# Optimization experiments

Hardware: AMD Instinct MI355X
Metric: run time of the kernel (lower is better)

## Reference

```python
import jax, jax.numpy as jnp
import numpy as np

WINDOW_SIZE = 11
SIGMA = 1.5
K2 = 0.03
PAD = WINDOW_SIZE // 2


def _gaussian_window(size, sigma):
    coords = np.arange(size, dtype=np.float32) - size // 2
    g = np.exp(-coords ** 2 / (2.0 * sigma ** 2))
    g = g / g.sum()
    w2d = np.outer(g, g)  # [size, size]
    return jnp.asarray(w2d[None, None], dtype=jnp.float32)  # [1,1,size,size]


def _blur(x, w):
    # x: [B,1,H,W], w: [1,1,k,k]; SAME zero padding, matches F.conv2d(padding=k//2)
    return jax.lax.conv_general_dilated(
        x, w, window_strides=(1, 1), padding=[(PAD, PAD), (PAD, PAD)],
        dimension_numbers=("NCHW", "OIHW", "NCHW"))


def setup_inputs() -> dict:
    key = jax.random.key(0)
    k1, k2 = jax.random.split(key)
    B, C, H, W = 32, 1, 512, 512
    inp = jax.random.uniform(k1, (B, C, H, W), dtype=jnp.float32)
    tgt = jax.random.uniform(k2, (B, C, H, W), dtype=jnp.float32)
    mask = jnp.ones((B, C, H, W), dtype=jnp.float32)
    window = _gaussian_window(WINDOW_SIZE, SIGMA)
    return {"input": inp, "target": tgt, "mask": mask, "window": window}


def reference(input, target, mask, window):
    # mask application (mask path is always exercised, matching the torch code)
    inp = input * mask
    tgt = target * mask

    mw = _blur(mask, window) + 1e-08  # blurred mask normalizer

    mu_i = _blur(inp, window) / mw
    mu_t = _blur(tgt, window) / mw

    sigma_i_sq = _blur(inp * inp, window) / mw - mu_i * mu_i
    sigma_t_sq = _blur(tgt * tgt, window) / mw - mu_t * mu_t
    sigma_it = _blur(inp * tgt, window) / mw - mu_i * mu_t

    L = jnp.maximum(jnp.max(inp), jnp.max(tgt))
    C2 = (K2 * L) ** 2
    C3 = C2 / 2.0

    sigma_i = jnp.sqrt(jax.nn.relu(sigma_i_sq) + 1e-12)
    sigma_t = jnp.sqrt(jax.nn.relu(sigma_t_sq) + 1e-12)

    structure_map = (sigma_it + C3) / (sigma_i * sigma_t + C3 + 1e-08)
    return 1.0 - jnp.mean(structure_map)
```

## Files before the change

### kernel.cpp

```cpp
#include <hip/hip_runtime.h>
#include <math.h>

#define H 512
#define W 512
#define TX 32
#define TY 32
#define SX 44
#define NPIX (32LL*512*512)

__device__ inline unsigned encf(float f) {
    unsigned u = __float_as_uint(f);
    return (u & 0x80000000u) ? ~u : (u | 0x80000000u);
}
__device__ inline float decf(unsigned e) {
    unsigned u = (e & 0x80000000u) ? (e ^ 0x80000000u) : ~e;
    return __uint_as_float(u);
}

__global__ __launch_bounds__(256) void maxred_kernel(
        const float* __restrict__ in, const float* __restrict__ tg,
        const float* __restrict__ mk, unsigned* __restrict__ mx) {
    const float4* in4 = (const float4*)in;
    const float4* tg4 = (const float4*)tg;
    const float4* mk4 = (const float4*)mk;
    long long n4 = NPIX / 4;
    long long idx = (long long)blockIdx.x * blockDim.x + threadIdx.x;
    long long stride = (long long)gridDim.x * blockDim.x;
    float ma = -INFINITY, mb = -INFINITY;
    for (long long i = idx; i < n4; i += stride) {
        float4 a = in4[i], b = tg4[i], c = mk4[i];
        ma = fmaxf(ma, fmaxf(fmaxf(a.x * c.x, a.y * c.y), fmaxf(a.z * c.z, a.w * c.w)));
        mb = fmaxf(mb, fmaxf(fmaxf(b.x * c.x, b.y * c.y), fmaxf(b.z * c.z, b.w * c.w)));
    }
    float m = fmaxf(ma, mb);
    #pragma unroll
    for (int off = 32; off; off >>= 1) m = fmaxf(m, __shfl_down(m, off, 64));
    __shared__ float smax[4];
    int lane = threadIdx.x & 63, wid = threadIdx.x >> 6;
    if (lane == 0) smax[wid] = m;
    __syncthreads();
    if (threadIdx.x == 0) {
        float r = fmaxf(fmaxf(smax[0], smax[1]), fmaxf(smax[2], smax[3]));
        atomicMax(mx, encf(r));
    }
}

__global__ __launch_bounds__(256, 4) void ssim_kernel(
        const float* __restrict__ in, const float* __restrict__ tg,
        const float* __restrict__ mk, const float* __restrict__ win,
        const unsigned* __restrict__ mxp, double* __restrict__ sum) {
    __shared__ __align__(16) float vch[6][TY][SX];
    __shared__ float gw[11];
    __shared__ float ssum[4];

    int t = threadIdx.x;
    if (t < 11) {
        float s = 0.f;
        #pragma unroll
        for (int j = 0; j < 11; j++) s += win[t * 11 + j];
        gw[t] = s;
    }
    float L = decf(*mxp);
    float C3 = 0.5f * (0.03f * L) * (0.03f * L);
    __syncthreads();

    float wk[11];
    #pragma unroll
    for (int k = 0; k < 11; k++)
        wk[k] = __uint_as_float(__builtin_amdgcn_readfirstlane(__float_as_uint(gw[k])));

    int img = blockIdx.z;
    int y0 = blockIdx.y * TY, x0 = blockIdx.x * TX;
    const size_t base = (size_t)img * H * W;
    const float* inb = in + base;
    const float* tgb = tg + base;
    const float* mkb = mk + base;

    if (t < 168) {
        int s = t / 42, cc = t - s * 42;
        int x = x0 - 5 + cc;
        bool inx = (unsigned)x < (unsigned)W;
        int xc = inx ? x : 0;
        float xs = inx ? 1.f : 0.f;
        int ybase = y0 + 8 * s - 5;
        float acc[6][8];
        #pragma unroll
        for (int ch = 0; ch < 6; ch++)
            #pragma unroll
            for (int u = 0; u < 8; u++) acc[ch][u] = 0.f;

        if (ybase >= 0 && ybase <= H - 18) {
            size_t g = (size_t)ybase * W + xc;
            #pragma unroll
            for (int j = 0; j < 18; j++) {
                float m = mkb[g], iv = inb[g], tv = tgb[g];
                g += W;
                float a = iv * m, b = tv * m;
                float v[6] = { m, a, b, a * a, b * b, a * b };
                #pragma unroll
                for (int u = 0; u < 8; u++) {
                    int k = j - u;
                    if (k >= 0 && k < 11) {
                        float w = wk[k];
                        #pragma unroll
                        for (int ch = 0; ch < 6; ch++)
                            acc[ch][u] = fmaf(w, v[ch], acc[ch][u]);
                    }
                }
            }
        } else {
            #pragma unroll
            for (int j = 0; j < 18; j++) {
                int y = ybase + j;
                bool yok = (unsigned)y < (unsigned)H;
                size_t g = (size_t)(yok ? y : 0) * W + xc;
                float sc = yok ? 1.f : 0.f;
                float m = mkb[g] * sc, iv = inb[g] * sc, tv = tgb[g] * sc;
                float a = iv * m, b = tv * m;
                float v[6] = { m, a, b, a * a, b * b, a * b };
                #pragma unroll
                for (int u = 0; u < 8; u++) {
                    int k = j - u;
                    if (k >= 0 && k < 11) {
                        float w = wk[k];
                        #pragma unroll
                        for (int ch = 0; ch < 6; ch++)
                            acc[ch][u] = fmaf(w, v[ch], acc[ch][u]);
                    }
                }
            }
        }
        #pragma unroll
        for (int u = 0; u < 8; u++) {
            int rr = 8 * s + u;
            #pragma unroll
            for (int ch = 0; ch < 6; ch++) vch[ch][rr][cc + 2] = acc[ch][u] * xs;
        }
    }
    __syncthreads();

    int r = t >> 3, c0 = (t & 7) << 2;
    float hs[6][4];
    #pragma unroll
    for (int ch = 0; ch < 6; ch++) {
        float Wl[16];
        #pragma unroll
        for (int q = 0; q < 4; q++) {
            float4 v = *(const float4*)&vch[ch][r][c0 + 4 * q];
            Wl[4 * q + 0] = v.x; Wl[4 * q + 1] = v.y;
            Wl[4 * q + 2] = v.z; Wl[4 * q + 3] = v.w;
        }
        #pragma unroll
        for (int u = 0; u < 4; u++) {
            float h = 0.f;
            #pragma unroll
            for (int k = 0; k < 11; k++) h = fmaf(wk[k], Wl[u + 2 + k], h);
            hs[ch][u] = h;
        }
    }

    float lsum = 0.f;
    #pragma unroll
    for (int u = 0; u < 4; u++) {
        float h1 = hs[1][u], h2 = hs[2][u];
        float mw = hs[0][u] + 1e-8f;
        float mw2 = mw * mw;
        float e12 = 1e-12f * mw2;
        float Xi = fmaxf(fmaf(hs[3][u], mw, -h1 * h1), 0.f) + e12;
        float Xt = fmaxf(fmaf(hs[4][u], mw, -h2 * h2), 0.f) + e12;
        float num = fmaf(hs[5][u], mw, -h1 * h2) + C3 * mw2;
        float den = __builtin_amdgcn_sqrtf(Xi * Xt) + (C3 + 1e-8f) * mw2;
        lsum += num * __builtin_amdgcn_rcpf(den);
    }

    #pragma unroll
    for (int off = 32; off; off >>= 1) lsum += __shfl_down(lsum, off, 64);
    int lane = t & 63, wid = t >> 6;
    if (lane == 0) ssum[wid] = lsum;
    __syncthreads();
    if (t == 0) {
        float tot = ssum[0] + ssum[1] + ssum[2] + ssum[3];
        atomicAdd(sum, (double)tot);
    }
}

__global__ void fin_kernel(const double* __restrict__ sum, float* __restrict__ out) {
    out[0] = 1.0f - (float)(*sum / (double)NPIX);
}

extern "C" void kernel_launch(void* const* d_in, const int* in_sizes, int n_in,
                              void* d_out, int out_size, void* d_ws, size_t ws_size,
                              hipStream_t stream) {
    const float* in  = (const float*)d_in[0];
    const float* tg  = (const float*)d_in[1];
    const float* mk  = (const float*)d_in[2];
    const float* win = (const float*)d_in[3];
    float* out = (float*)d_out;

    double*   dsum = (double*)d_ws;
    unsigned* dmax = (unsigned*)((char*)d_ws + 8);

    hipMemsetAsync(d_ws, 0, 12, stream);
    maxred_kernel<<<2048, 256, 0, stream>>>(in, tg, mk, dmax);
    ssim_kernel<<<dim3(16, 16, 32), 256, 0, stream>>>(in, tg, mk, win, dmax, dsum);
    fin_kernel<<<1, 1, 0, stream>>>(dsum, out);
}
```

Baseline: 158.2 us.

## Stage raw input tiles in shared memory with coalesced loads before vertical blur

The kernel now cooperatively loads a 42x42 halo tile of input, target and mask into shared memory with coalesced row-major loads and zero padding applied at load time. The vertical pass then reads from LDS instead of doing strided column global loads. The same LDS buffer is reused for the vertical-pass outputs, which needs an extra barrier. Occupancy hint is raised from 4 to 5 blocks per CU, and the horizontal pass reads float2 from a 42-stride layout. The aim is better global coalescing and less divergent boundary handling, at the cost of more shared memory traffic and an extra synchronisation.

```diff
diff --git a/kernel.cpp b/kernel.cpp
--- a/kernel.cpp
+++ b/kernel.cpp
@@ -3,10 +3,11 @@
 
 #define H 512
 #define W 512
-#define TX 32
-#define TY 32
-#define SX 44
 #define NPIX (32LL*512*512)
+
+#define RSTR 45
+#define RAWF(a,r,c)  uni[(a)*(42*RSTR) + (r)*RSTR + (c)]
+#define VCHF(ch,r,c) uni[(ch)*(32*42) + (r)*42 + (c)]
 
 __device__ inline unsigned encf(float f) {
     unsigned u = __float_as_uint(f);
@@ -45,11 +46,11 @@
     }
 }
 
-__global__ __launch_bounds__(256, 4) void ssim_kernel(
+__global__ __launch_bounds__(256, 5) void ssim_kernel(
         const float* __restrict__ in, const float* __restrict__ tg,
         const float* __restrict__ mk, const float* __restrict__ win,
         const unsigned* __restrict__ mxp, double* __restrict__ sum) {
-    __shared__ __align__(16) float vch[6][TY][SX];
+    __shared__ __align__(16) float uni[8072];
     __shared__ float gw[11];
     __shared__ float ssum[4];
 
@@ -62,6 +63,34 @@
     }
     float L = decf(*mxp);
     float C3 = 0.5f * (0.03f * L) * (0.03f * L);
+
+    int img = blockIdx.z;
+    int y0 = blockIdx.y * 32, x0 = blockIdx.x * 32;
+    const size_t base = (size_t)img * H * W;
+    const float* __restrict__ inb = in + base;
+    const float* __restrict__ tgb = tg + base;
+    const float* __restrict__ mkb = mk + base;
+
+    {
+        int y0m5 = y0 - 5, x0m5 = x0 - 5;
+        #pragma unroll
+        for (int a = 0; a < 3; a++) {
+            const float* __restrict__ src = (a == 0) ? inb : (a == 1) ? tgb : mkb;
+            #pragma unroll
+            for (int i = 0; i < 7; i++) {
+                int idx = t + 256 * i;
+                int row = idx / 42;
+                int col = idx - row * 42;
+                if (row < 42) {
+                    int y = y0m5 + row, x = x0m5 + col;
+                    bool ok = ((unsigned)y < (unsigned)H) && ((unsigned)x < (unsigned)W);
+                    size_t g = ok ? ((size_t)y * W + x) : 0;
+                    float v = src[g];
+                    RAWF(a, row, col) = ok ? v : 0.f;
+                }
+            }
+        }
+    }
     __syncthreads();
 
     float wk[11];
@@ -69,72 +98,41 @@
     for (int k = 0; k < 11; k++)
         wk[k] = __uint_as_float(__builtin_amdgcn_readfirstlane(__float_as_uint(gw[k])));
 
-    int img = blockIdx.z;
-    int y0 = blockIdx.y * TY, x0 = blockIdx.x * TX;
-    const size_t base = (size_t)img * H * W;
-    const float* inb = in + base;
-    const float* tgb = tg + base;
-    const float* mkb = mk + base;
-
-    if (t < 168) {
-        int s = t / 42, cc = t - s * 42;
-        int x = x0 - 5 + cc;
-        bool inx = (unsigned)x < (unsigned)W;
-        int xc = inx ? x : 0;
-        float xs = inx ? 1.f : 0.f;
-        int ybase = y0 + 8 * s - 5;
-        float acc[6][8];
+    int sNo = t / 42, cc = t - sNo * 42;
+    bool vact = t < 168;
+    float acc[6][8];
+    if (vact) {
         #pragma unroll
         for (int ch = 0; ch < 6; ch++)
             #pragma unroll
             for (int u = 0; u < 8; u++) acc[ch][u] = 0.f;
-
-        if (ybase >= 0 && ybase <= H - 18) {
-            size_t g = (size_t)ybase * W + xc;
-            #pragma unroll
-            for (int j = 0; j < 18; j++) {
-                float m = mkb[g], iv = inb[g], tv = tgb[g];
-                g += W;
-                float a = iv * m, b = tv * m;
-                float v[6] = { m, a, b, a * a, b * b, a * b };
-                #pragma unroll
-                for (int u = 0; u < 8; u++) {
-                    int k = j - u;
-                    if (k >= 0 && k < 11) {
-                        float w = wk[k];
-                        #pragma unroll
-                        for (int ch = 0; ch < 6; ch++)
-                            acc[ch][u] = fmaf(w, v[ch], acc[ch][u]);
-                    }
+        #pragma unroll
+        for (int j = 0; j < 18; j++) {
+            int rr = 8 * sNo + j;
+            float iv = RAWF(0, rr, cc);
+            float tv = RAWF(1, rr, cc);
+            float m  = RAWF(2, rr, cc);
+            float a = iv * m, b = tv * m;
+            float v[6] = { m, a, b, a * a, b * b, a * b };
+            #pragma unroll
+            for (int u = 0; u < 8; u++) {
+                int k = j - u;
+                if (k >= 0 && k < 11) {
+                    float w = wk[k];
+                    #pragma unroll
+                    for (int ch = 0; ch < 6; ch++)
+                        acc[ch][u] = fmaf(w, v[ch], acc[ch][u]);
                 }
             }
-        } else {
-            #pragma unroll
-            for (int j = 0; j < 18; j++) {
-                int y = ybase + j;
-                bool yok = (unsigned)y < (unsigned)H;
-                size_t g = (size_t)(yok ? y : 0) * W + xc;
-                float sc = yok ? 1.f : 0.f;
-                float m = mkb[g] * sc, iv = inb[g] * sc, tv = tgb[g] * sc;
-                float a = iv * m, b = tv * m;
-                float v[6] = { m, a, b, a * a, b * b, a * b };
-                #pragma unroll
-                for (int u = 0; u < 8; u++) {
-                    int k = j - u;
-                    if (k >= 0 && k < 11) {
-                        float w = wk[k];
-                        #pragma unroll
-                        for (int ch = 0; ch < 6; ch++)
-                            acc[ch][u] = fmaf(w, v[ch], acc[ch][u]);
-                    }
-                }
-            }
-        }
+        }
+    }
+    __syncthreads();
+    if (vact) {
         #pragma unroll
         for (int u = 0; u < 8; u++) {
-            int rr = 8 * s + u;
-            #pragma unroll
-            for (int ch = 0; ch < 6; ch++) vch[ch][rr][cc + 2] = acc[ch][u] * xs;
+            int rr = 8 * sNo + u;
+            #pragma unroll
+            for (int ch = 0; ch < 6; ch++) VCHF(ch, rr, cc) = acc[ch][u];
         }
     }
     __syncthreads();
@@ -143,18 +141,17 @@
     float hs[6][4];
     #pragma unroll
     for (int ch = 0; ch < 6; ch++) {
-        float Wl[16];
-        #pragma unroll
-        for (int q = 0; q < 4; q++) {
-            float4 v = *(const float4*)&vch[ch][r][c0 + 4 * q];
-            Wl[4 * q + 0] = v.x; Wl[4 * q + 1] = v.y;
-            Wl[4 * q + 2] = v.z; Wl[4 * q + 3] = v.w;
+        float Wl[14];
+        #pragma unroll
+        for (int q = 0; q < 7; q++) {
+            float2 v = *(const float2*)&VCHF(ch, r, c0 + 2 * q);
+            Wl[2 * q] = v.x; Wl[2 * q + 1] = v.y;
         }
         #pragma unroll
         for (int u = 0; u < 4; u++) {
             float h = 0.f;
             #pragma unroll
-            for (int k = 0; k < 11; k++) h = fmaf(wk[k], Wl[u + 2 + k], h);
+            for (int k = 0; k < 11; k++) h = fmaf(wk[k], Wl[u + k], h);
             hs[ch][u] = h;
         }
     }
```

Result: slower. 166.4 us (+5.2%).

## Make each wave own an 8-row strip to drop block-wide barriers in SSIM

Applied to the files above, without the earlier changes.

Restructures the SSIM tile so each of the four waves computes the vertical blur for its own 8 rows using 42 lanes, stores it to a per-wave LDS slice, and runs the horizontal pass from that slice after only a wave-level barrier. This removes two block-wide __syncthreads and lets all four waves do vertical work, where before only 168 of 256 threads were active. Window weights now come through a cross-lane shuffle instead of shared memory. LDS reads change from float4 to float2 because of the 42-float stride. The x-boundary zeroing moves into the mask scale, and 22 lanes per wave still sit idle during the vertical pass.

```diff
diff --git a/kernel.cpp b/kernel.cpp
--- a/kernel.cpp
+++ b/kernel.cpp
@@ -3,10 +3,10 @@
 
 #define H 512
 #define W 512
-#define TX 32
-#define TY 32
-#define SX 44
 #define NPIX (32LL*512*512)
+
+#define VSTR 42
+#define VCH(wid,ch,u,c) uni[(wid)*2016 + (ch)*336 + (u)*VSTR + (c)]
 
 __device__ inline unsigned encf(float f) {
     unsigned u = __float_as_uint(f);
@@ -49,40 +49,41 @@
         const float* __restrict__ in, const float* __restrict__ tg,
         const float* __restrict__ mk, const float* __restrict__ win,
         const unsigned* __restrict__ mxp, double* __restrict__ sum) {
-    __shared__ __align__(16) float vch[6][TY][SX];
-    __shared__ float gw[11];
+    __shared__ __align__(16) float uni[8064];
     __shared__ float ssum[4];
 
     int t = threadIdx.x;
-    if (t < 11) {
-        float s = 0.f;
-        #pragma unroll
-        for (int j = 0; j < 11; j++) s += win[t * 11 + j];
-        gw[t] = s;
-    }
+    int lane = t & 63, wid = t >> 6;
+
+    float rs = 0.f;
+    if (lane < 11) {
+        #pragma unroll
+        for (int j = 0; j < 11; j++) rs += win[lane * 11 + j];
+    }
+    float wk[11];
+    #pragma unroll
+    for (int k = 0; k < 11; k++)
+        wk[k] = __uint_as_float(__builtin_amdgcn_readfirstlane(
+                    __float_as_uint(__shfl(rs, k, 64))));
+
     float L = decf(*mxp);
     float C3 = 0.5f * (0.03f * L) * (0.03f * L);
-    __syncthreads();
-
-    float wk[11];
-    #pragma unroll
-    for (int k = 0; k < 11; k++)
-        wk[k] = __uint_as_float(__builtin_amdgcn_readfirstlane(__float_as_uint(gw[k])));
 
     int img = blockIdx.z;
-    int y0 = blockIdx.y * TY, x0 = blockIdx.x * TX;
+    int y0w = blockIdx.y * 32 + wid * 8;
+    int x0  = blockIdx.x * 32;
     const size_t base = (size_t)img * H * W;
-    const float* inb = in + base;
-    const float* tgb = tg + base;
-    const float* mkb = mk + base;
-
-    if (t < 168) {
-        int s = t / 42, cc = t - s * 42;
-        int x = x0 - 5 + cc;
+    const float* __restrict__ inb = in + base;
+    const float* __restrict__ tgb = tg + base;
+    const float* __restrict__ mkb = mk + base;
+
+    if (lane < 42) {
+        int x = x0 - 5 + lane;
         bool inx = (unsigned)x < (unsigned)W;
         int xc = inx ? x : 0;
         float xs = inx ? 1.f : 0.f;
-        int ybase = y0 + 8 * s - 5;
+        int ybase = y0w - 5;
+
         float acc[6][8];
         #pragma unroll
         for (int ch = 0; ch < 6; ch++)
@@ -93,7 +94,7 @@
             size_t g = (size_t)ybase * W + xc;
             #pragma unroll
             for (int j = 0; j < 18; j++) {
-                float m = mkb[g], iv = inb[g], tv = tgb[g];
+                float iv = inb[g], tv = tgb[g], m = mkb[g] * xs;
                 g += W;
                 float a = iv * m, b = tv * m;
                 float v[6] = { m, a, b, a * a, b * b, a * b };
@@ -114,8 +115,8 @@
                 int y = ybase + j;
                 bool yok = (unsigned)y < (unsigned)H;
                 size_t g = (size_t)(yok ? y : 0) * W + xc;
-                float sc = yok ? 1.f : 0.f;
-                float m = mkb[g] * sc, iv = inb[g] * sc, tv = tgb[g] * sc;
+                float sc = yok ? xs : 0.f;
+                float iv = inb[g], tv = tgb[g], m = mkb[g] * sc;
                 float a = iv * m, b = tv * m;
                 float v[6] = { m, a, b, a * a, b * b, a * b };
                 #pragma unroll
@@ -131,30 +132,30 @@
             }
         }
         #pragma unroll
-        for (int u = 0; u < 8; u++) {
-            int rr = 8 * s + u;
-            #pragma unroll
-            for (int ch = 0; ch < 6; ch++) vch[ch][rr][cc + 2] = acc[ch][u] * xs;
-        }
-    }
-    __syncthreads();
-
-    int r = t >> 3, c0 = (t & 7) << 2;
+        for (int u = 0; u < 8; u++)
+            #pragma unroll
+            for (int ch = 0; ch < 6; ch++) VCH(wid, ch, u, lane) = acc[ch][u];
+    }
+
+    __builtin_amdgcn_wave_barrier();
+    asm volatile("s_waitcnt lgkmcnt(0)" ::: "memory");
+    __builtin_amdgcn_sched_barrier(0);
+
+    int r = lane >> 3, c0 = (lane & 7) << 2;
     float hs[6][4];
     #pragma unroll
     for (int ch = 0; ch < 6; ch++) {
-        float Wl[16];
-        #pragma unroll
-        for (int q = 0; q < 4; q++) {
-            float4 v = *(const float4*)&vch[ch][r][c0 + 4 * q];
-            Wl[4 * q + 0] = v.x; Wl[4 * q + 1] = v.y;
-            Wl[4 * q + 2] = v.z; Wl[4 * q + 3] = v.w;
+        float Wl[14];
+        #pragma unroll
+        for (int q = 0; q < 7; q++) {
+            float2 v = *(const float2*)&VCH(wid, ch, r, c0 + 2 * q);
+            Wl[2 * q] = v.x; Wl[2 * q + 1] = v.y;
         }
         #pragma unroll
         for (int u = 0; u < 4; u++) {
             float h = 0.f;
             #pragma unroll
-            for (int k = 0; k < 11; k++) h = fmaf(wk[k], Wl[u + 2 + k], h);
+            for (int k = 0; k < 11; k++) h = fmaf(wk[k], Wl[u + k], h);
             hs[ch][u] = h;
         }
     }
@@ -175,7 +176,6 @@
 
     #pragma unroll
     for (int off = 32; off; off >>= 1) lsum += __shfl_down(lsum, off, 64);
-    int lane = t & 63, wid = t >> 6;
     if (lane == 0) ssum[wid] = lsum;
     __syncthreads();
     if (t == 0) {
```

After: 159.9 us. No clear change (+1.1%).
